# Kernel tuning notes

Measured on AMD Instinct MI355X. Metric: run time of the kernel, lower is better.

The kernel has to match this reference:

```python
import jax, jax.numpy as jnp
import numpy as np

HEADS = 8
NEG_SLOPE = 0.2


def _layer_norm(x, g, b, eps=1e-5):
    mu = x.mean(-1, keepdims=True)
    var = ((x - mu) ** 2).mean(-1, keepdims=True)
    return (x - mu) / jnp.sqrt(var + eps) * g + b


def setup_inputs() -> dict:
    key = jax.random.key(0)
    ks = jax.random.split(key, 24)
    N, E, H, L = 512, 260000, 256, 4
    s = 0.05
    return dict(
        x=jax.random.normal(ks[0], (N, 1), jnp.float32),
        edge_index=jax.random.randint(ks[1], (2, E), 0, N),
        edge_attr=jax.random.uniform(ks[2], (E, 3), jnp.float32),
        emb_W=jax.random.normal(ks[3], (1, H)) * s,
        emb_b=jnp.zeros((H,)),
        Wl=jax.random.normal(ks[4], (L, H, H)) * s,
        bl=jnp.zeros((L, H)),
        Wr=jax.random.normal(ks[5], (L, H, H)) * s,
        br=jnp.zeros((L, H)),
        We=jax.random.normal(ks[6], (L, 3, H)) * s,
        att=jax.random.normal(ks[7], (L, HEADS, H // HEADS)) * s,
        gb=jnp.zeros((L, H)),
        ln_g=jnp.ones((L, H)),
        ln_b=jnp.zeros((L, H)),
        p1_W=jax.random.normal(ks[8], (2 * H, H)) * s,
        p1_b=jnp.zeros((H,)),
        p2_W=jax.random.normal(ks[9], (H, H // 2)) * s,
        p2_b=jnp.zeros((H // 2,)),
        p3_W=jax.random.normal(ks[10], (H // 2, 1)) * s,
        p3_b=jnp.zeros((1,)),
        v1_W=jax.random.normal(ks[11], (2 * H, H)) * s,
        v1_b=jnp.zeros((H,)),
        v2_W=jax.random.normal(ks[12], (H, 1)) * s,
        v2_b=jnp.zeros((1,)),
        coupling=jnp.asarray(1.0, jnp.float32),
    )


def reference(x, edge_index, edge_attr, emb_W, emb_b, Wl, bl, Wr, br, We, att,
              gb, ln_g, ln_b, p1_W, p1_b, p2_W, p2_b, p3_W, p3_b,
              v1_W, v1_b, v2_W, v2_b, coupling):
    N = x.shape[0]
    E = edge_attr.shape[0]
    L = Wl.shape[0]
    C = Wl.shape[-1] // HEADS
    src, dst = edge_index[0], edge_index[1]

    # PyG GATv2Conv adds self-loops with edge_attr fill_value='mean'
    # (mean of incoming edge_attr per destination node).
    sums = jax.ops.segment_sum(edge_attr, dst, num_segments=N)
    cnt = jax.ops.segment_sum(jnp.ones((E,), edge_attr.dtype), dst, num_segments=N)
    self_attr = sums / jnp.maximum(cnt, 1.0)[:, None]
    loop = jnp.arange(N)
    src_f = jnp.concatenate([src, loop])            # [E+N]
    dst_f = jnp.concatenate([dst, loop])
    ea_f = jnp.concatenate([edge_attr, self_attr])  # [E+N, 3]

    h = x @ emb_W + emb_b                           # [N, H]
    for l in range(L):
        res = h
        xl = (h @ Wl[l] + bl[l]).reshape(N, HEADS, C)
        xr = (h @ Wr[l] + br[l]).reshape(N, HEADS, C)
        ee = (ea_f @ We[l]).reshape(-1, HEADS, C)
        # GATv2 scoring: leaky_relu(x_l[src]+x_r[dst]+edge) . att
        m = jax.nn.leaky_relu(xl[src_f] + xr[dst_f] + ee, NEG_SLOPE)
        alpha = jnp.einsum('ehc,hc->eh', m, att[l])
        amax = jax.ops.segment_max(alpha, dst_f, num_segments=N)
        alpha = jnp.exp(alpha - amax[dst_f])
        denom = jax.ops.segment_sum(alpha, dst_f, num_segments=N)
        alpha = alpha / denom[dst_f]
        out = jax.ops.segment_sum(xl[src_f] * alpha[..., None], dst_f,
                                  num_segments=N).reshape(N, HEADS * C) + gb[l]
        h = jax.nn.relu(_layer_norm(out + res, ln_g[l], ln_b[l]))

    # graph-level representation (single graph, batch=None branch)
    graph_repr = jnp.concatenate([h.mean(0, keepdims=True),
                                  h.max(0, keepdims=True)], axis=1)  # [1, 2H]

    # all-pairs edge representations (i < j)
    iu, ju = jnp.triu_indices(N, k=1)
    er = jnp.concatenate([h[iu], h[ju]], axis=1)    # [N(N-1)/2, 2H]
    p = jax.nn.relu(er @ p1_W + p1_b)
    p = jax.nn.relu(p @ p2_W + p2_b)
    policy_logits = (p @ p3_W + p3_b).squeeze(-1)   # [N(N-1)/2]

    v = jax.nn.relu(graph_repr @ v1_W + v1_b)
    value = (v @ v2_W + v2_b).squeeze(-1)           # [1]

    # Potts energy: per-color degree-squared approximation of triangles
    colors = jnp.argmax(edge_attr, axis=1)
    energy = jnp.asarray(0.0, h.dtype)
    for c in (1, 2):
        w = (colors == c).astype(h.dtype)
        deg = (jax.ops.segment_sum(w, src, num_segments=N)
               + jax.ops.segment_sum(w, dst, num_segments=N))
        energy = energy + (deg ** 2).sum() / (2.0 * N)
    energy = energy * coupling

    return policy_logits, value, energy
```

## Files before the change

kernel.cpp:

```cpp
#include <hip/hip_runtime.h>
#include <math.h>

#define HDIM 256
#define NHEADS 8
#define NEG 0.2f
#define SEG 4
#define STRIDE 768

typedef float f32x4 __attribute__((ext_vector_type(4)));
typedef _Float16 f16x8 __attribute__((ext_vector_type(8)));
typedef __fp16 fp16v2 __attribute__((ext_vector_type(2)));

union H8 { f16x8 v8; fp16v2 v2[4]; _Float16 h[8]; };

#if __has_builtin(__builtin_amdgcn_fdot2)
#define FDOT2(a, b, c) __builtin_amdgcn_fdot2((a), (b), (c), false)
#else
__device__ __forceinline__ float FDOT2(fp16v2 a, fp16v2 b, float c) {
  return fmaf((float)a[1], (float)b[1], fmaf((float)a[0], (float)b[0], c));
}
#endif

__global__ __launch_bounds__(256) void zero_k(int* __restrict__ p) {
  p[blockIdx.x * 256 + threadIdx.x] = 0;
}

__global__ __launch_bounds__(256) void build_csr(
    const int* __restrict__ ei, const float* __restrict__ ea, int E, int CH,
    int* __restrict__ rcnt, float* __restrict__ asum, int* __restrict__ dcol,
    float4* __restrict__ csr) {
  __shared__ int   lcnt[512];
  __shared__ float ls0[512], ls1[512], ls2[512];
  __shared__ int   lcol[1024];
  __shared__ int   lbase[512];
  int t = threadIdx.x, b = blockIdx.x;
  for (int n = t; n < 512; n += 256) {
    lcnt[n] = 0; ls0[n] = 0.f; ls1[n] = 0.f; ls2[n] = 0.f;
    lcol[n] = 0; lcol[512 + n] = 0;
  }
  __syncthreads();
  int e0 = b * CH, e1 = min(E, e0 + CH);

  int nd[4], ns[4], slot[4];
  float va0[4], va1[4], va2[4];
#pragma unroll
  for (int k = 0; k < 4; ++k) {
    int e = e0 + t + (k << 8);
    bool v = e < e1;
    if (v) {
      int src = ei[e], dst = ei[E + e];
      float a0 = ea[3*e], a1 = ea[3*e+1], a2 = ea[3*e+2];
      nd[k] = dst; ns[k] = src; va0[k] = a0; va1[k] = a1; va2[k] = a2;
      slot[k] = atomicAdd(&lcnt[dst], 1);
      atomicAdd(&ls0[dst], a0);
      atomicAdd(&ls1[dst], a1);
      atomicAdd(&ls2[dst], a2);
      int idx = 0; float best = a0;
      if (a1 > best) { best = a1; idx = 1; }
      if (a2 > best) { idx = 2; }
      if (idx) {
        int o = (idx - 1) << 9;
        atomicAdd(&lcol[o + src], 1);
        atomicAdd(&lcol[o + dst], 1);
      }
    } else {
      nd[k] = -1;
    }
  }
  __syncthreads();
  for (int n = t; n < 512; n += 256) {
    int c = lcnt[n];
    if (c) {
      lbase[n] = atomicAdd(&rcnt[n], c);
      atomicAdd(&asum[n],        ls0[n]);
      atomicAdd(&asum[512 + n],  ls1[n]);
      atomicAdd(&asum[1024 + n], ls2[n]);
    }
    int c0 = lcol[n], c1 = lcol[512 + n];
    if (c0) atomicAdd(&dcol[n], c0);
    if (c1) atomicAdd(&dcol[512 + n], c1);
  }
  __syncthreads();
#pragma unroll
  for (int k = 0; k < 4; ++k) {
    if (nd[k] >= 0) {
      int pos = nd[k]*STRIDE + 1 + lbase[nd[k]] + slot[k];
      csr[pos] = make_float4(va0[k], va1[k], va2[k], __int_as_float(ns[k]));
    }
  }
}

__global__ __launch_bounds__(512) void csr_finish(
    const int* __restrict__ rcnt, const float* __restrict__ asum,
    const int* __restrict__ dcol, int N,
    float4* __restrict__ csr, const float* __restrict__ coupling,
    float* __restrict__ eout) {
  int t = threadIdx.x;
  float e = 0.f;
  if (t < N) {
    int c = rcnt[t];
    float inv = 1.f / fmaxf((float)c, 1.f);
    csr[(size_t)t*STRIDE] = make_float4(asum[t]*inv, asum[512 + t]*inv,
                                        asum[1024 + t]*inv, __int_as_float(t));
    float d1 = (float)dcol[t], d2 = (float)dcol[512 + t];
    e = d1*d1 + d2*d2;
  }
#pragma unroll
  for (int off = 1; off < 64; off <<= 1) e += __shfl_xor(e, off);
  __shared__ float wred[8];
  if ((t & 63) == 0) wred[t >> 6] = e;
  __syncthreads();
  if (t == 0) {
    float s = 0.f;
#pragma unroll
    for (int i = 0; i < 8; ++i) s += wred[i];
    eout[0] = coupling[0] * s / (2.f * (float)N);
  }
}

__global__ __launch_bounds__(256) void w_prep_all(
    const float* __restrict__ Wl, const float* __restrict__ Wr,
    const float* __restrict__ p1W, const float* __restrict__ W2,
    unsigned short* __restrict__ dst, unsigned short* __restrict__ W2h) {
  int gid = blockIdx.x * 256 + threadIdx.x;
  if (gid < 10*65536) {
    int s = gid >> 16, e = gid & 65535;
    int k = e >> 8, n = e & 255;
    const float* src = (s < 4) ? (Wl + (size_t)s*65536)
                     : (s < 8) ? (Wr + (size_t)(s-4)*65536)
                               : (p1W + (size_t)(s-8)*65536);
    int c = k >> 5, quad = (k >> 3) & 3, kj = k & 7;
    int nt = n >> 4, nl = n & 15;
    int lane = quad*16 + nl;
    _Float16 hv = (_Float16)src[(size_t)k*256 + n];
    dst[(size_t)s*65536 + ((nt*8 + c)*512 + lane*8 + kj)] = *(unsigned short*)&hv;
  } else {
    int e = gid - 10*65536;
    int k = e >> 7, n = e & 127;
    int c = k >> 5, kq = (k >> 3) & 3, kj = k & 7;
    int nt = n >> 4, nl = n & 15;
    int lane = kq*16 + nl;
    _Float16 hv = (_Float16)W2[(size_t)k*128 + n];
    W2h[(size_t)(((c*8 + nt)*64 + lane)*8 + kj)] = *(unsigned short*)&hv;
  }
}

__global__ __launch_bounds__(256) void dual_gemm_mfma(
    const float* __restrict__ Hm,
    const float* __restrict__ x, const float* __restrict__ embW,
    const float* __restrict__ embb,
    const unsigned short* __restrict__ W1h, const unsigned short* __restrict__ W2h,
    const float* __restrict__ b1, const float* __restrict__ b2,
    float* __restrict__ o1, unsigned short* __restrict__ o1h,
    float* __restrict__ o2, unsigned short* __restrict__ o2h) {
  int bx = blockIdx.x, by = blockIdx.y;
  int t = threadIdx.x, w = t >> 6, l = t & 63;
  int quad = l >> 4, nl = l & 15;
  int mt = bx*4 + w;

  const unsigned short* Wh; const float* bias; float* o; unsigned short* oh; int nt;
  bool first = (by < 16);
  if (first) { Wh = W1h; bias = b1; o = o1; oh = o1h; nt = by; }
  else       { Wh = W2h; bias = b2; o = o2; oh = o2h; nt = by - 16; }

  int row = mt*16 + nl;
  const float* Ar = Hm ? (Hm + (size_t)row*HDIM + quad*8) : nullptr;
  float xm = Hm ? 0.f : x[row];
  f32x4 acc = (f32x4){0.f, 0.f, 0.f, 0.f};

#pragma unroll
  for (int c = 0; c < 8; ++c) {
    float4 a0, a1;
    if (Hm) {
      a0 = *(const float4*)(Ar + c*32);
      a1 = *(const float4*)(Ar + c*32 + 4);
    } else {
      int kb = c*32 + quad*8;
      float4 e0 = *(const float4*)(embW + kb);
      float4 e1 = *(const float4*)(embW + kb + 4);
      float4 c0 = *(const float4*)(embb + kb);
      float4 c1 = *(const float4*)(embb + kb + 4);
      a0 = make_float4(fmaf(xm, e0.x, c0.x), fmaf(xm, e0.y, c0.y),
                       fmaf(xm, e0.z, c0.z), fmaf(xm, e0.w, c0.w));
      a1 = make_float4(fmaf(xm, e1.x, c1.x), fmaf(xm, e1.y, c1.y),
                       fmaf(xm, e1.z, c1.z), fmaf(xm, e1.w, c1.w));
    }
    union { f16x8 v8; fp16v2 v2[4]; } u;
    u.v2[0] = __builtin_amdgcn_cvt_pkrtz(a0.x, a0.y);
    u.v2[1] = __builtin_amdgcn_cvt_pkrtz(a0.z, a0.w);
    u.v2[2] = __builtin_amdgcn_cvt_pkrtz(a1.x, a1.y);
    u.v2[3] = __builtin_amdgcn_cvt_pkrtz(a1.z, a1.w);
    f16x8 bfrag = *(const f16x8*)(Wh + (size_t)((nt*8 + c)*512 + l*8));
    acc = __builtin_amdgcn_mfma_f32_16x16x32_f16(u.v8, bfrag, acc, 0, 0, 0);
  }

  int colg = nt*16 + nl;
  float bv = bias ? bias[colg] : 0.f;
#pragma unroll
  for (int r = 0; r < 4; ++r) {
    float val = acc[r] + bv;
    size_t idx = (size_t)(mt*16 + quad*4 + r)*HDIM + colg;
    if (o) o[idx] = val;
    if (oh) {
      _Float16 hv = (_Float16)val;
      oh[idx] = *(unsigned short*)&hv;
    }
  }
}

__global__ __launch_bounds__(256) void attn_gather(
    const unsigned short* __restrict__ xlh, const unsigned short* __restrict__ xrh,
    const float4* __restrict__ csr, const int* __restrict__ rcnt,
    const float* __restrict__ We, const float* __restrict__ att,
    float* __restrict__ pm, float* __restrict__ pl, float* __restrict__ pacc) {
  int nb = blockIdx.x;
  int n = nb >> 2, sgm = nb & (SEG - 1);
  int t = threadIdx.x;
  int g = t >> 5, l = t & 31, hd = l >> 2, qd = l & 3;
  int cb = hd*32 + qd*8;

  union H8 w0u, w1u, w2u, avu;
#pragma unroll
  for (int p = 0; p < 4; ++p) {
    w0u.v2[p] = __builtin_amdgcn_cvt_pkrtz(We[cb + 2*p],          We[cb + 2*p + 1]);
    w1u.v2[p] = __builtin_amdgcn_cvt_pkrtz(We[HDIM + cb + 2*p],   We[HDIM + cb + 2*p + 1]);
    w2u.v2[p] = __builtin_amdgcn_cvt_pkrtz(We[2*HDIM + cb + 2*p], We[2*HDIM + cb + 2*p + 1]);
    avu.v2[p] = __builtin_amdgcn_cvt_pkrtz(att[cb + 2*p],         att[cb + 2*p + 1]);
  }
  f16x8 xr8 = *(const f16x8*)(xrh + (size_t)n*HDIM + cb);

  int base = n * STRIDE;
  int len = rcnt[n] + 1;
  int s0 = base + ((len * sgm) >> 2);
  int s1 = base + ((len * (sgm + 1)) >> 2);

  float mh = -INFINITY, lh = 0.f;
  float acc[8] = {0.f,0.f,0.f,0.f,0.f,0.f,0.f,0.f};

  int idx = s0 + g;
  if (idx < s1) {
    float4 rec = csr[idx];
    int idx1 = idx + 8;
    float4 rec1 = csr[idx1 < s1 ? idx1 : base];
    union H8 cur, nxt;
    cur.v8 = *(const f16x8*)(xlh + (size_t)__float_as_int(rec.w)*HDIM + cb);
    while (idx < s1) {
      int idx2 = idx1 + 8;
      float4 rec2 = csr[idx2 < s1 ? idx2 : base];
      nxt.v8 = *(const f16x8*)(xlh +
                (size_t)__float_as_int(rec1.w)*HDIM + cb);
      _Float16 hx = (_Float16)rec.x, hy = (_Float16)rec.y, hz = (_Float16)rec.z;
      f16x8 s = cur.v8 + xr8;
      s = s + w0u.v8 * hx;
      s = s + w1u.v8 * hy;
      s = s + w2u.v8 * hz;
      union H8 m;
      m.v8 = __builtin_elementwise_max(s, s * (_Float16)NEG);
      float partial = FDOT2(m.v2[3], avu.v2[3],
                      FDOT2(m.v2[2], avu.v2[2],
                      FDOT2(m.v2[1], avu.v2[1],
                      FDOT2(m.v2[0], avu.v2[0], 0.f))));
      partial += __shfl_xor(partial, 1);
      partial += __shfl_xor(partial, 2);
      if (partial - mh > 8.f) {
        float sc = __expf(mh - partial);
        lh *= sc;
#pragma unroll
        for (int j = 0; j < 8; ++j) acc[j] *= sc;
        mh = partial;
      }
      float pw = __expf(partial - mh);
      lh += pw;
#pragma unroll
      for (int j = 0; j < 8; ++j) acc[j] = fmaf(pw, (float)cur.h[j], acc[j]);
      rec = rec1; rec1 = rec2; cur.v8 = nxt.v8;
      idx = idx1; idx1 = idx2;
    }
  }

  __shared__ float lacc[8][HDIM];
  __shared__ float lm[8][NHEADS];
  __shared__ float llv[8][NHEADS];
#pragma unroll
  for (int j = 0; j < 8; ++j) lacc[g][cb + j] = acc[j];
  if (qd == 0) { lm[g][hd] = mh; llv[g][hd] = lh; }
  __syncthreads();

  int c = t, hh = c >> 5;
  float M = -INFINITY;
#pragma unroll
  for (int g2 = 0; g2 < 8; ++g2) M = fmaxf(M, lm[g2][hh]);
  float L = 0.f, o = 0.f;
#pragma unroll
  for (int g2 = 0; g2 < 8; ++g2) {
    float e2 = __expf(lm[g2][hh] - M);
    L = fmaf(llv[g2][hh], e2, L);
    o = fmaf(lacc[g2][c], e2, o);
  }
  pacc[(size_t)nb*HDIM + c] = o;
  if ((c & 31) == 0) {
    pm[nb*NHEADS + hh] = M;
    pl[nb*NHEADS + hh] = L;
  }
}

__global__ __launch_bounds__(256) void attn_merge(
    const float* __restrict__ pm, const float* __restrict__ pl,
    const float* __restrict__ pacc,
    const float* __restrict__ gb, const float* __restrict__ lng,
    const float* __restrict__ lnb,
    const float* __restrict__ h_in,
    const float* __restrict__ x, const float* __restrict__ embW,
    const float* __restrict__ embb,
    float* __restrict__ h_out) {
  int n = blockIdx.x, t = threadIdx.x;
  int c = t, hh = c >> 5;
  float M = -INFINITY;
#pragma unroll
  for (int s = 0; s < SEG; ++s) M = fmaxf(M, pm[(n*SEG + s)*NHEADS + hh]);
  float L = 0.f, o = 0.f;
#pragma unroll
  for (int s = 0; s < SEG; ++s) {
    float e2 = __expf(pm[(n*SEG + s)*NHEADS + hh] - M);
    L = fmaf(pl[(n*SEG + s)*NHEADS + hh], e2, L);
    o = fmaf(pacc[(size_t)(n*SEG + s)*HDIM + c], e2, o);
  }
  float hi = h_in ? h_in[(size_t)n*HDIM + c] : fmaf(x[n], embW[c], embb[c]);
  float val = o / L + gb[c] + hi;

  float s1 = val, s2 = val * val;
#pragma unroll
  for (int off = 1; off < 64; off <<= 1) {
    s1 += __shfl_xor(s1, off);
    s2 += __shfl_xor(s2, off);
  }
  __shared__ float rs1[4], rs2[4];
  if ((t & 63) == 0) { rs1[t >> 6] = s1; rs2[t >> 6] = s2; }
  __syncthreads();
  float S1 = rs1[0] + rs1[1] + rs1[2] + rs1[3];
  float S2 = rs2[0] + rs2[1] + rs2[2] + rs2[3];
  float mu = S1 * (1.f/HDIM);
  float var = S2 * (1.f/HDIM) - mu * mu;
  float y = (val - mu) * rsqrtf(var + 1e-5f);
  y = fmaf(y, lng[c], lnb[c]);
  h_out[(size_t)n*HDIM + c] = fmaxf(y, 0.f);
}

__global__ __launch_bounds__(256, 4) void pair_mfma_kernel(
    const unsigned short* __restrict__ Ah, const unsigned short* __restrict__ Bh,
    const unsigned short* __restrict__ W2h,
    const float* __restrict__ b2, const float* __restrict__ W3,
    const float* __restrict__ b3, float* __restrict__ out, int N) {
  int bb = blockIdx.x;
  int half = bb & 1;
  int b = bb >> 1, ti = 0, rem = 32;
  while (b >= rem) { b -= rem; ti++; rem--; }
  int tj = ti + b;
  int i0 = ti * 16 + half * 8;
  int j0 = tj * 16;

  int t = threadIdx.x;
  int w = t >> 6, l = t & 63;
  int quad = l >> 4, nl = l & 15;

  float b2v[8], w3v[8];
#pragma unroll
  for (int nt = 0; nt < 8; ++nt) {
    b2v[nt] = b2[nt*16 + nl];
    w3v[nt] = W3[nt*16 + nl];
  }

  const unsigned short* Brow = Bh + (size_t)(j0 + nl) * HDIM;
  const unsigned short* Arow0 = Ah + (size_t)(i0 + w*2) * HDIM;
  const f16x8 zv = {};

  f32x4 acc[2][8];
#pragma unroll
  for (int a2 = 0; a2 < 2; ++a2)
#pragma unroll
    for (int nt = 0; nt < 8; ++nt) acc[a2][nt] = (f32x4){0.f,0.f,0.f,0.f};

  for (int c = 0; c < 8; ++c) {
    int kb = c*32 + quad*8;
    f16x8 bv = *(const f16x8*)(Brow + kb);

    f16x8 afrag[2];
#pragma unroll
    for (int a2 = 0; a2 < 2; ++a2) {
      f16x8 av = *(const f16x8*)(Arow0 + (size_t)a2*HDIM + kb);
      afrag[a2] = __builtin_elementwise_max(av + bv, zv);
    }

#pragma unroll
    for (int nt = 0; nt < 8; ++nt) {
      f16x8 bfrag = *(const f16x8*)(W2h + (size_t)(((c*8 + nt)*64 + l) * 8));
#pragma unroll
      for (int a2 = 0; a2 < 2; ++a2)
        acc[a2][nt] = __builtin_amdgcn_mfma_f32_16x16x32_f16(
            afrag[a2], bfrag, acc[a2][nt], 0, 0, 0);
    }
  }

  float b3v = b3[0];
#pragma unroll
  for (int a2 = 0; a2 < 2; ++a2) {
    int i = i0 + w*2 + a2;
#pragma unroll
    for (int r = 0; r < 4; ++r) {
      float s = 0.f;
#pragma unroll
      for (int nt = 0; nt < 8; ++nt)
        s = fmaf(fmaxf(acc[a2][nt][r] + b2v[nt], 0.f), w3v[nt], s);
      s += __shfl_xor(s, 1);
      s += __shfl_xor(s, 2);
      s += __shfl_xor(s, 4);
      s += __shfl_xor(s, 8);
      if (nl == 0) {
        int j = j0 + quad*4 + r;
        if (i < j)
          out[(size_t)i*(2*N - i - 1)/2 + (j - i - 1)] = s + b3v;
      }
    }
  }
}

__global__ __launch_bounds__(256) void pool_kernel(
    const float* __restrict__ h, float* __restrict__ psums,
    float* __restrict__ pmaxs) {
  int g = blockIdx.x, t = threadIdx.x;
  float s = 0.f, m = -INFINITY;
#pragma unroll
  for (int r = 0; r < 16; ++r) {
    float v = h[(size_t)(g*16 + r)*HDIM + t];
    s += v; m = fmaxf(m, v);
  }
  psums[g*HDIM + t] = s;
  pmaxs[g*HDIM + t] = m;
}

__global__ __launch_bounds__(256) void value1_kernel(
    const float* __restrict__ psums, const float* __restrict__ pmaxs,
    const float* __restrict__ v1W, float* __restrict__ vpart, int N) {
  int b = blockIdx.x, t = threadIdx.x;
  int k0 = b * 16;
  int kk = t >> 4, g = t & 15;
  __shared__ float repr16[16];
  int k = k0 + kk;
  float v;
  if (k < HDIM) {
    v = psums[g*HDIM + k] + psums[(g + 16)*HDIM + k];
    v += __shfl_xor(v, 1); v += __shfl_xor(v, 2);
    v += __shfl_xor(v, 4); v += __shfl_xor(v, 8);
    if (g == 0) repr16[kk] = v / (float)N;
  } else {
    int kc = k - HDIM;
    v = fmaxf(pmaxs[g*HDIM + kc], pmaxs[(g + 16)*HDIM + kc]);
    v = fmaxf(v, __shfl_xor(v, 1)); v = fmaxf(v, __shfl_xor(v, 2));
    v = fmaxf(v, __shfl_xor(v, 4)); v = fmaxf(v, __shfl_xor(v, 8));
    if (g == 0) repr16[kk] = v;
  }
  __syncthreads();
  float pv = 0.f;
#pragma unroll
  for (int q = 0; q < 16; ++q)
    pv = fmaf(repr16[q], v1W[(size_t)(k0 + q)*HDIM + t], pv);
  vpart[b*HDIM + t] = pv;
}

__global__ __launch_bounds__(256) void value2_kernel(
    const float* __restrict__ vpart, const float* __restrict__ v1b,
    const float* __restrict__ v2W, const float* __restrict__ v2b,
    float* __restrict__ out) {
  int t = threadIdx.x;
  float a = 0.f;
#pragma unroll
  for (int g = 0; g < 32; ++g) a += vpart[g*HDIM + t];
  a = fmaxf(a + v1b[t], 0.f);
  float pv = a * v2W[t];
#pragma unroll
  for (int off = 1; off < 64; off <<= 1) pv += __shfl_xor(pv, off);
  __shared__ float wsum[4];
  if ((t & 63) == 0) wsum[t >> 6] = pv;
  __syncthreads();
  if (t == 0) out[0] = wsum[0] + wsum[1] + wsum[2] + wsum[3] + v2b[0];
}

extern "C" void kernel_launch(void* const* d_in, const int* in_sizes, int n_in,
                              void* d_out, int out_size, void* d_ws, size_t ws_size,
                              hipStream_t stream) {
  const float* x    = (const float*)d_in[0];
  const int*   ei   = (const int*)  d_in[1];
  const float* ea   = (const float*)d_in[2];
  const float* embW = (const float*)d_in[3];
  const float* embb = (const float*)d_in[4];
  const float* Wl   = (const float*)d_in[5];
  const float* bl   = (const float*)d_in[6];
  const float* Wr   = (const float*)d_in[7];
  const float* br   = (const float*)d_in[8];
  const float* We   = (const float*)d_in[9];
  const float* att  = (const float*)d_in[10];
  const float* gb   = (const float*)d_in[11];
  const float* lng  = (const float*)d_in[12];
  const float* lnb  = (const float*)d_in[13];
  const float* p1W  = (const float*)d_in[14];
  const float* p1b  = (const float*)d_in[15];
  const float* p2W  = (const float*)d_in[16];
  const float* p2b  = (const float*)d_in[17];
  const float* p3W  = (const float*)d_in[18];
  const float* p3b  = (const float*)d_in[19];
  const float* v1W  = (const float*)d_in[20];
  const float* v1b  = (const float*)d_in[21];
  const float* v2W  = (const float*)d_in[22];
  const float* v2b  = (const float*)d_in[23];
  const float* coup = (const float*)d_in[24];

  int N = in_sizes[0];
  int E = in_sizes[2] / 3;
  float* out = (float*)d_out;
  size_t P = (size_t)N*(N-1)/2;

  char* w = (char*)d_ws;
  int*    rcnt = (int*)   (w + 0);
  float*  asum = (float*) (w + 2048);
  int*    dcol = (int*)   (w + 8192);
  float*  plS  = (float*) (w + 12288);
  float*  plM  = (float*) (w + 45056);
  float*  vprt = (float*) (w + 77824);
  float4* csr  = (float4*)(w + 110592);
  float* hA  = (float*)(w + 6402048);
  float* hB  = (float*)(w + 6926336);
  unsigned short* xlh = (unsigned short*)(w + 7450624);
  unsigned short* xrh = (unsigned short*)(w + 7712768);
  unsigned short* Abh = (unsigned short*)(w + 7974912);
  unsigned short* Bbh = (unsigned short*)(w + 8237056);
  unsigned short* W2h = (unsigned short*)(w + 8499200);
  unsigned short* Whall = (unsigned short*)(w + 8564736);
  float*  pmv  = (float*) (w + 9875456);
  float*  plv  = (float*) (w + 9940992);
  float*  pacc = (float*) (w + 10006528);

  zero_k<<<12, 256, 0, stream>>>(rcnt);
  int nbB = (E + 1023) >> 10;
  build_csr<<<nbB, 256, 0, stream>>>(ei, ea, E, 1024, rcnt, asum, dcol, csr);
  csr_finish<<<1, 512, 0, stream>>>(rcnt, asum, dcol, N, csr, coup, out + P + 1);
  w_prep_all<<<2688, 256, 0, stream>>>(Wl, Wr, p1W, p2W, Whall, W2h);

  float* hin = nullptr;
  float* hout = hB;
  for (int l = 0; l < 4; ++l) {
    dual_gemm_mfma<<<dim3(8, 32), 256, 0, stream>>>(hin, x, embW, embb,
        Whall + (size_t)l*65536, Whall + (size_t)(4 + l)*65536,
        bl + l*HDIM, br + l*HDIM,
        (float*)nullptr, xlh, (float*)nullptr, xrh);
    attn_gather<<<N*SEG, 256, 0, stream>>>(xlh, xrh, csr, rcnt,
        We + (size_t)l*3*HDIM, att + (size_t)l*HDIM, pmv, plv, pacc);
    attn_merge<<<N, 256, 0, stream>>>(pmv, plv, pacc,
        gb + (size_t)l*HDIM, lng + (size_t)l*HDIM, lnb + (size_t)l*HDIM,
        hin, x, embW, embb, hout);
    hin = hout;
    hout = (hout == hB) ? hA : hB;
  }

  dual_gemm_mfma<<<dim3(8, 32), 256, 0, stream>>>(hin, x, embW, embb,
      Whall + (size_t)8*65536, Whall + (size_t)9*65536,
      p1b, (const float*)nullptr,
      (float*)nullptr, Abh, (float*)nullptr, Bbh);

  pair_mfma_kernel<<<1056, 256, 0, stream>>>(Abh, Bbh, W2h, p2b, p3W, p3b, out, N);

  pool_kernel<<<32, 256, 0, stream>>>(hin, plS, plM);
  value1_kernel<<<32, 256, 0, stream>>>(plS, plM, v1W, vprt, N);
  value2_kernel<<<1, 256, 0, stream>>>(vprt, v1b, v2W, v2b, out + P);
}
```

Before: 298.1 us.

## Fuse whole pipeline into persistent megakernel with software grid barriers

Replaces the sequence of roughly twenty kernel launches with one persistent kernel of 512 blocks. Stages are separated by an atomic-counter grid barrier, and independent work (CSR build with weight prep, CSR finish with the first GEMM, pooling with the final GEMM) is co-scheduled within a stage. The attention gather no longer splits each node into 4 segments plus a separate merge; one block now handles a whole node with a deeper prefetch pipeline and applies LayerNorm inline. This removes launch gaps and the partial-result round trips, but gives less parallelism per node in the gather, and the barrier relies on all 512 blocks being resident at once.

```diff
diff --git a/kernel.cpp b/kernel.cpp
--- a/kernel.cpp
+++ b/kernel.cpp
@@ -4,8 +4,8 @@
 #define HDIM 256
 #define NHEADS 8
 #define NEG 0.2f
-#define SEG 4
 #define STRIDE 768
+#define GRID 512
 
 typedef float f32x4 __attribute__((ext_vector_type(4)));
 typedef _Float16 f16x8 __attribute__((ext_vector_type(8)));
@@ -25,29 +25,39 @@
   p[blockIdx.x * 256 + threadIdx.x] = 0;
 }
 
-__global__ __launch_bounds__(256) void build_csr(
-    const int* __restrict__ ei, const float* __restrict__ ea, int E, int CH,
-    int* __restrict__ rcnt, float* __restrict__ asum, int* __restrict__ dcol,
-    float4* __restrict__ csr) {
-  __shared__ int   lcnt[512];
-  __shared__ float ls0[512], ls1[512], ls2[512];
-  __shared__ int   lcol[1024];
-  __shared__ int   lbase[512];
-  int t = threadIdx.x, b = blockIdx.x;
+__device__ __forceinline__ void gbar(int* bar, int target) {
+  __syncthreads();
+  if (threadIdx.x == 0) {
+    __hip_atomic_fetch_add(bar, 1, __ATOMIC_ACQ_REL, __HIP_MEMORY_SCOPE_AGENT);
+    while (__hip_atomic_load(bar, __ATOMIC_RELAXED, __HIP_MEMORY_SCOPE_AGENT) < target)
+      __builtin_amdgcn_s_sleep(2);
+    (void)__hip_atomic_load(bar, __ATOMIC_ACQUIRE, __HIP_MEMORY_SCOPE_AGENT);
+  }
+  __syncthreads();
+}
+
+__device__ __forceinline__ void build_work(int b, const int* ei, const float* ea,
+    int E, int* rcnt, float* asum, int* dcol, float4* csr, char* SMEM) {
+  int*   lcnt = (int*)SMEM;
+  float* ls0  = (float*)(SMEM + 2048);
+  float* ls1  = (float*)(SMEM + 4096);
+  float* ls2  = (float*)(SMEM + 6144);
+  int*   lcol = (int*)(SMEM + 8192);
+  int*   lbase= (int*)(SMEM + 12288);
+  int t = threadIdx.x;
   for (int n = t; n < 512; n += 256) {
     lcnt[n] = 0; ls0[n] = 0.f; ls1[n] = 0.f; ls2[n] = 0.f;
     lcol[n] = 0; lcol[512 + n] = 0;
   }
   __syncthreads();
-  int e0 = b * CH, e1 = min(E, e0 + CH);
+  int e0 = b << 10, e1 = min(E, e0 + 1024);
 
   int nd[4], ns[4], slot[4];
   float va0[4], va1[4], va2[4];
 #pragma unroll
   for (int k = 0; k < 4; ++k) {
     int e = e0 + t + (k << 8);
-    bool v = e < e1;
-    if (v) {
+    if (e < e1) {
       int src = ei[e], dst = ei[E + e];
       float a0 = ea[3*e], a1 = ea[3*e+1], a2 = ea[3*e+2];
       nd[k] = dst; ns[k] = src; va0[k] = a0; va1[k] = a1; va2[k] = a2;
@@ -90,39 +100,10 @@
   }
 }
 
-__global__ __launch_bounds__(512) void csr_finish(
-    const int* __restrict__ rcnt, const float* __restrict__ asum,
-    const int* __restrict__ dcol, int N,
-    float4* __restrict__ csr, const float* __restrict__ coupling,
-    float* __restrict__ eout) {
-  int t = threadIdx.x;
-  float e = 0.f;
-  if (t < N) {
-    int c = rcnt[t];
-    float inv = 1.f / fmaxf((float)c, 1.f);
-    csr[(size_t)t*STRIDE] = make_float4(asum[t]*inv, asum[512 + t]*inv,
-                                        asum[1024 + t]*inv, __int_as_float(t));
-    float d1 = (float)dcol[t], d2 = (float)dcol[512 + t];
-    e = d1*d1 + d2*d2;
-  }
-#pragma unroll
-  for (int off = 1; off < 64; off <<= 1) e += __shfl_xor(e, off);
-  __shared__ float wred[8];
-  if ((t & 63) == 0) wred[t >> 6] = e;
-  __syncthreads();
-  if (t == 0) {
-    float s = 0.f;
-#pragma unroll
-    for (int i = 0; i < 8; ++i) s += wred[i];
-    eout[0] = coupling[0] * s / (2.f * (float)N);
-  }
-}
-
-__global__ __launch_bounds__(256) void w_prep_all(
-    const float* __restrict__ Wl, const float* __restrict__ Wr,
-    const float* __restrict__ p1W, const float* __restrict__ W2,
-    unsigned short* __restrict__ dst, unsigned short* __restrict__ W2h) {
-  int gid = blockIdx.x * 256 + threadIdx.x;
+__device__ __forceinline__ void wprep_work(int wid, const float* Wl,
+    const float* Wr, const float* p1W, const float* W2,
+    unsigned short* dst, unsigned short* W2h) {
+  int gid = wid * 256 + (int)threadIdx.x;
   if (gid < 10*65536) {
     int s = gid >> 16, e = gid & 65535;
     int k = e >> 8, n = e & 255;
@@ -145,23 +126,41 @@
   }
 }
 
-__global__ __launch_bounds__(256) void dual_gemm_mfma(
-    const float* __restrict__ Hm,
-    const float* __restrict__ x, const float* __restrict__ embW,
-    const float* __restrict__ embb,
-    const unsigned short* __restrict__ W1h, const unsigned short* __restrict__ W2h,
-    const float* __restrict__ b1, const float* __restrict__ b2,
-    float* __restrict__ o1, unsigned short* __restrict__ o1h,
-    float* __restrict__ o2, unsigned short* __restrict__ o2h) {
-  int bx = blockIdx.x, by = blockIdx.y;
+__device__ __forceinline__ void csrfin_work(int half, const int* rcnt,
+    const float* asum, const int* dcol, int N, float4* csr, float* epart,
+    char* SMEM) {
+  float* er = (float*)SMEM;
+  int t = threadIdx.x;
+  int n = half*256 + t;
+  float e = 0.f;
+  if (n < N) {
+    int c = rcnt[n];
+    float inv = 1.f / fmaxf((float)c, 1.f);
+    csr[(size_t)n*STRIDE] = make_float4(asum[n]*inv, asum[512 + n]*inv,
+                                        asum[1024 + n]*inv, __int_as_float(n));
+    float d1 = (float)dcol[n], d2 = (float)dcol[512 + n];
+    e = d1*d1 + d2*d2;
+  }
+#pragma unroll
+  for (int off = 1; off < 64; off <<= 1) e += __shfl_xor(e, off);
+  if ((t & 63) == 0) er[t >> 6] = e;
+  __syncthreads();
+  if (t == 0) epart[half] = er[0] + er[1] + er[2] + er[3];
+}
+
+__device__ __forceinline__ void gemm_work(int wid, const float* Hm,
+    const float* x, const float* embW, const float* embb,
+    const unsigned short* W1h, const unsigned short* W2h_,
+    const float* b1, const float* b2,
+    unsigned short* o1h, unsigned short* o2h) {
+  int bx = wid & 7, by = wid >> 3;
   int t = threadIdx.x, w = t >> 6, l = t & 63;
   int quad = l >> 4, nl = l & 15;
   int mt = bx*4 + w;
 
-  const unsigned short* Wh; const float* bias; float* o; unsigned short* oh; int nt;
-  bool first = (by < 16);
-  if (first) { Wh = W1h; bias = b1; o = o1; oh = o1h; nt = by; }
-  else       { Wh = W2h; bias = b2; o = o2; oh = o2h; nt = by - 16; }
+  const unsigned short* Wh; const float* bias; unsigned short* oh; int nt;
+  if (by < 16) { Wh = W1h; bias = b1; oh = o1h; nt = by; }
+  else         { Wh = W2h_; bias = b2; oh = o2h; nt = by - 16; }
 
   int row = mt*16 + nl;
   const float* Ar = Hm ? (Hm + (size_t)row*HDIM + quad*8) : nullptr;
@@ -200,22 +199,29 @@
   for (int r = 0; r < 4; ++r) {
     float val = acc[r] + bv;
     size_t idx = (size_t)(mt*16 + quad*4 + r)*HDIM + colg;
-    if (o) o[idx] = val;
-    if (oh) {
-      _Float16 hv = (_Float16)val;
-      oh[idx] = *(unsigned short*)&hv;
-    }
-  }
-}
-
-__global__ __launch_bounds__(256) void attn_gather(
-    const unsigned short* __restrict__ xlh, const unsigned short* __restrict__ xrh,
-    const float4* __restrict__ csr, const int* __restrict__ rcnt,
-    const float* __restrict__ We, const float* __restrict__ att,
-    float* __restrict__ pm, float* __restrict__ pl, float* __restrict__ pacc) {
-  int nb = blockIdx.x;
-  int n = nb >> 2, sgm = nb & (SEG - 1);
+    _Float16 hv = (_Float16)val;
+    oh[idx] = *(unsigned short*)&hv;
+  }
+}
+
+__device__ __forceinline__ void gather_merge_work(int n,
+    const unsigned short* xlh, const unsigned short* xrh,
+    const float4* csr, const int* rcnt,
+    const float* We, const float* att,
+    const float* gb, const float* lng, const float* lnb,
+    const float* h_in, const float* x, const float* embW, const float* embb,
+    float* h_out, const float* epart, const float* coup, float* eout,
+    int N, char* SMEM) {
+  float* lacc = (float*)SMEM;
+  float* lm   = (float*)(SMEM + 8192);
+  float* llv  = (float*)(SMEM + 8448);
+  float* rs1  = (float*)(SMEM + 8704);
+  float* rs2  = (float*)(SMEM + 8720);
+
   int t = threadIdx.x;
+  if (eout && t == 0)
+    eout[0] = coup[0] * (epart[0] + epart[1]) / (2.f * (float)N);
+
   int g = t >> 5, l = t & 31, hd = l >> 2, qd = l & 3;
   int cb = hd*32 + qd*8;
 
@@ -230,25 +236,25 @@
   f16x8 xr8 = *(const f16x8*)(xrh + (size_t)n*HDIM + cb);
 
   int base = n * STRIDE;
-  int len = rcnt[n] + 1;
-  int s0 = base + ((len * sgm) >> 2);
-  int s1 = base + ((len * (sgm + 1)) >> 2);
+  int send = base + rcnt[n] + 1;
 
   float mh = -INFINITY, lh = 0.f;
   float acc[8] = {0.f,0.f,0.f,0.f,0.f,0.f,0.f,0.f};
 
-  int idx = s0 + g;
-  if (idx < s1) {
-    float4 rec = csr[idx];
-    int idx1 = idx + 8;
-    float4 rec1 = csr[idx1 < s1 ? idx1 : base];
-    union H8 cur, nxt;
+  int idx = base + g;
+  if (idx < send) {
+    int i1 = idx + 8, i2 = idx + 16;
+    float4 rec  = csr[idx];
+    float4 rec1 = csr[i1 < send ? i1 : base];
+    float4 rec2 = csr[i2 < send ? i2 : base];
+    union H8 cur, nxt, nx2;
     cur.v8 = *(const f16x8*)(xlh + (size_t)__float_as_int(rec.w)*HDIM + cb);
-    while (idx < s1) {
-      int idx2 = idx1 + 8;
-      float4 rec2 = csr[idx2 < s1 ? idx2 : base];
-      nxt.v8 = *(const f16x8*)(xlh +
-                (size_t)__float_as_int(rec1.w)*HDIM + cb);
+    nxt.v8 = *(const f16x8*)(xlh + (size_t)__float_as_int(rec1.w)*HDIM + cb);
+    while (idx < send) {
+      int i3 = i2 + 8;
+      float4 rec3 = csr[i3 < send ? i3 : base];
+      nx2.v8 = *(const f16x8*)(xlh +
+                (size_t)__float_as_int(rec2.w)*HDIM + cb);
       _Float16 hx = (_Float16)rec.x, hy = (_Float16)rec.y, hz = (_Float16)rec.z;
       f16x8 s = cur.v8 + xr8;
       s = s + w0u.v8 * hx;
@@ -273,69 +279,38 @@
       lh += pw;
 #pragma unroll
       for (int j = 0; j < 8; ++j) acc[j] = fmaf(pw, (float)cur.h[j], acc[j]);
-      rec = rec1; rec1 = rec2; cur.v8 = nxt.v8;
-      idx = idx1; idx1 = idx2;
-    }
-  }
-
-  __shared__ float lacc[8][HDIM];
-  __shared__ float lm[8][NHEADS];
-  __shared__ float llv[8][NHEADS];
-#pragma unroll
-  for (int j = 0; j < 8; ++j) lacc[g][cb + j] = acc[j];
-  if (qd == 0) { lm[g][hd] = mh; llv[g][hd] = lh; }
+      rec = rec1; rec1 = rec2; rec2 = rec3;
+      cur.v8 = nxt.v8; nxt.v8 = nx2.v8;
+      idx = i1; i1 = i2; i2 = i3;
+    }
+  }
+
+#pragma unroll
+  for (int j = 0; j < 8; ++j) lacc[g*HDIM + cb + j] = acc[j];
+  if (qd == 0) { lm[g*NHEADS + hd] = mh; llv[g*NHEADS + hd] = lh; }
   __syncthreads();
 
   int c = t, hh = c >> 5;
   float M = -INFINITY;
 #pragma unroll
-  for (int g2 = 0; g2 < 8; ++g2) M = fmaxf(M, lm[g2][hh]);
+  for (int g2 = 0; g2 < 8; ++g2) M = fmaxf(M, lm[g2*NHEADS + hh]);
   float L = 0.f, o = 0.f;
 #pragma unroll
   for (int g2 = 0; g2 < 8; ++g2) {
-    float e2 = __expf(lm[g2][hh] - M);
-    L = fmaf(llv[g2][hh], e2, L);
-    o = fmaf(lacc[g2][c], e2, o);
-  }
-  pacc[(size_t)nb*HDIM + c] = o;
-  if ((c & 31) == 0) {
-    pm[nb*NHEADS + hh] = M;
-    pl[nb*NHEADS + hh] = L;
-  }
-}
-
-__global__ __launch_bounds__(256) void attn_merge(
-    const float* __restrict__ pm, const float* __restrict__ pl,
-    const float* __restrict__ pacc,
-    const float* __restrict__ gb, const float* __restrict__ lng,
-    const float* __restrict__ lnb,
-    const float* __restrict__ h_in,
-    const float* __restrict__ x, const float* __restrict__ embW,
-    const float* __restrict__ embb,
-    float* __restrict__ h_out) {
-  int n = blockIdx.x, t = threadIdx.x;
-  int c = t, hh = c >> 5;
-  float M = -INFINITY;
-#pragma unroll
-  for (int s = 0; s < SEG; ++s) M = fmaxf(M, pm[(n*SEG + s)*NHEADS + hh]);
-  float L = 0.f, o = 0.f;
-#pragma unroll
-  for (int s = 0; s < SEG; ++s) {
-    float e2 = __expf(pm[(n*SEG + s)*NHEADS + hh] - M);
-    L = fmaf(pl[(n*SEG + s)*NHEADS + hh], e2, L);
-    o = fmaf(pacc[(size_t)(n*SEG + s)*HDIM + c], e2, o);
+    float e2 = __expf(lm[g2*NHEADS + hh] - M);
+    L = fmaf(llv[g2*NHEADS + hh], e2, L);
+    o = fmaf(lacc[g2*HDIM + c], e2, o);
   }
   float hi = h_in ? h_in[(size_t)n*HDIM + c] : fmaf(x[n], embW[c], embb[c]);
   float val = o / L + gb[c] + hi;
 
-  float s1 = val, s2 = val * val;
+  float vs = val, vq = val * val;
 #pragma unroll
   for (int off = 1; off < 64; off <<= 1) {
-    s1 += __shfl_xor(s1, off);
-    s2 += __shfl_xor(s2, off);
-  }
-  __shared__ float rs1[4], rs2[4];
-  if ((t & 63) == 0) { rs1[t >> 6] = s1; rs2[t >> 6] = s2; }
+    vs += __shfl_xor(vs, off);
+    vq += __shfl_xor(vq, off);
+  }
+  if ((t & 63) == 0) { rs1[t >> 6] = vs; rs2[t >> 6] = vq; }
   __syncthreads();
   float S1 = rs1[0] + rs1[1] + rs1[2] + rs1[3];
   float S2 = rs2[0] + rs2[1] + rs2[2] + rs2[3];
@@ -346,12 +321,10 @@
   h_out[(size_t)n*HDIM + c] = fmaxf(y, 0.f);
 }
 
-__global__ __launch_bounds__(256, 4) void pair_mfma_kernel(
-    const unsigned short* __restrict__ Ah, const unsigned short* __restrict__ Bh,
-    const unsigned short* __restrict__ W2h,
-    const float* __restrict__ b2, const float* __restrict__ W3,
-    const float* __restrict__ b3, float* __restrict__ out, int N) {
-  int bb = blockIdx.x;
+__device__ __forceinline__ void pair_work(int bb,
+    const unsigned short* Ah, const unsigned short* Bh,
+    const unsigned short* W2h, const float* b2, const float* W3,
+    const float* b3, float* out, int N) {
   int half = bb & 1;
   int b = bb >> 1, ti = 0, rem = 32;
   while (b >= rem) { b -= rem; ti++; rem--; }
@@ -424,10 +397,9 @@
   }
 }
 
-__global__ __launch_bounds__(256) void pool_kernel(
-    const float* __restrict__ h, float* __restrict__ psums,
-    float* __restrict__ pmaxs) {
-  int g = blockIdx.x, t = threadIdx.x;
+__device__ __forceinline__ void pool_work(int g, const float* h,
+    float* psums, float* pmaxs) {
+  int t = threadIdx.x;
   float s = 0.f, m = -INFINITY;
 #pragma unroll
   for (int r = 0; r < 16; ++r) {
@@ -438,51 +410,119 @@
   pmaxs[g*HDIM + t] = m;
 }
 
-__global__ __launch_bounds__(256) void value1_kernel(
-    const float* __restrict__ psums, const float* __restrict__ pmaxs,
-    const float* __restrict__ v1W, float* __restrict__ vpart, int N) {
-  int b = blockIdx.x, t = threadIdx.x;
-  int k0 = b * 16;
-  int kk = t >> 4, g = t & 15;
-  __shared__ float repr16[16];
-  int k = k0 + kk;
-  float v;
-  if (k < HDIM) {
-    v = psums[g*HDIM + k] + psums[(g + 16)*HDIM + k];
-    v += __shfl_xor(v, 1); v += __shfl_xor(v, 2);
-    v += __shfl_xor(v, 4); v += __shfl_xor(v, 8);
-    if (g == 0) repr16[kk] = v / (float)N;
-  } else {
-    int kc = k - HDIM;
-    v = fmaxf(pmaxs[g*HDIM + kc], pmaxs[(g + 16)*HDIM + kc]);
-    v = fmaxf(v, __shfl_xor(v, 1)); v = fmaxf(v, __shfl_xor(v, 2));
-    v = fmaxf(v, __shfl_xor(v, 4)); v = fmaxf(v, __shfl_xor(v, 8));
-    if (g == 0) repr16[kk] = v;
-  }
-  __syncthreads();
-  float pv = 0.f;
-#pragma unroll
-  for (int q = 0; q < 16; ++q)
-    pv = fmaf(repr16[q], v1W[(size_t)(k0 + q)*HDIM + t], pv);
-  vpart[b*HDIM + t] = pv;
-}
-
-__global__ __launch_bounds__(256) void value2_kernel(
-    const float* __restrict__ vpart, const float* __restrict__ v1b,
+__device__ __forceinline__ void value_work(int q, const float* psums,
+    const float* pmaxs, const float* v1W, const float* v1b,
+    const float* v2W, float* out_val, int N, char* SMEM) {
+  float* repr = (float*)SMEM;
+  float* vred = (float*)(SMEM + 2048);
+  int t = threadIdx.x;
+  float s = 0.f, m = -INFINITY;
+#pragma unroll 8
+  for (int g = 0; g < 32; ++g) {
+    s += psums[g*HDIM + t];
+    m = fmaxf(m, pmaxs[g*HDIM + t]);
+  }
+  repr[t] = s / (float)N;
+  repr[256 + t] = m;
+  __syncthreads();
+  int cc = t & 63, kk = t >> 6;
+  int c = q*64 + cc;
+  float p = 0.f;
+#pragma unroll 8
+  for (int k = kk*128; k < kk*128 + 128; ++k)
+    p = fmaf(repr[k], v1W[(size_t)k*HDIM + c], p);
+  vred[kk*64 + cc] = p;
+  __syncthreads();
+  if (t < 64) {
+    float a = vred[t] + vred[64 + t] + vred[128 + t] + vred[192 + t] + v1b[c];
+    a = fmaxf(a, 0.f);
+    float pd = a * v2W[c];
+#pragma unroll
+    for (int off = 1; off < 64; off <<= 1) pd += __shfl_xor(pd, off);
+    if (t == 0) atomicAdd(out_val, pd);
+  }
+}
+
+__global__ __launch_bounds__(256, 2) void mega(
+    const float* __restrict__ x, const int* __restrict__ ei,
+    const float* __restrict__ ea,
+    const float* __restrict__ embW, const float* __restrict__ embb,
+    const float* __restrict__ Wl, const float* __restrict__ bl,
+    const float* __restrict__ Wr, const float* __restrict__ br,
+    const float* __restrict__ We, const float* __restrict__ att,
+    const float* __restrict__ gb, const float* __restrict__ lng,
+    const float* __restrict__ lnb,
+    const float* __restrict__ p1W, const float* __restrict__ p1b,
+    const float* __restrict__ p2W, const float* __restrict__ p2b,
+    const float* __restrict__ p3W, const float* __restrict__ p3b,
+    const float* __restrict__ v1W, const float* __restrict__ v1b,
     const float* __restrict__ v2W, const float* __restrict__ v2b,
-    float* __restrict__ out) {
-  int t = threadIdx.x;
-  float a = 0.f;
-#pragma unroll
-  for (int g = 0; g < 32; ++g) a += vpart[g*HDIM + t];
-  a = fmaxf(a + v1b[t], 0.f);
-  float pv = a * v2W[t];
-#pragma unroll
-  for (int off = 1; off < 64; off <<= 1) pv += __shfl_xor(pv, off);
-  __shared__ float wsum[4];
-  if ((t & 63) == 0) wsum[t >> 6] = pv;
-  __syncthreads();
-  if (t == 0) out[0] = wsum[0] + wsum[1] + wsum[2] + wsum[3] + v2b[0];
+    const float* __restrict__ coup,
+    int* rcnt, float* asum, int* dcol, float* epart,
+    float4* csr, float* hA, float* hB,
+    unsigned short* xlh, unsigned short* xrh,
+    unsigned short* Abh, unsigned short* Bbh,
+    unsigned short* W2h, unsigned short* Whall,
+    float* psums, float* pmaxs, int* bar,
+    float* out, int N, int E) {
+  __shared__ __align__(16) char SMEM[14336];
+  size_t P = (size_t)N*(N-1)/2;
+  int ph = 0;
+
+  {
+    int WB = (E + 1023) >> 10;
+    for (int wid = blockIdx.x; wid < WB + 2688; wid += GRID) {
+      if (wid < WB) build_work(wid, ei, ea, E, rcnt, asum, dcol, csr, SMEM);
+      else          wprep_work(wid - WB, Wl, Wr, p1W, p2W, Whall, W2h);
+    }
+  }
+  ++ph; gbar(bar, ph * GRID);
+
+  for (int wid = blockIdx.x; wid < 258; wid += GRID) {
+    if (wid < 2) csrfin_work(wid, rcnt, asum, dcol, N, csr, epart, SMEM);
+    else gemm_work(wid - 2, nullptr, x, embW, embb,
+                   Whall, Whall + (size_t)4*65536, bl, br, xlh, xrh);
+  }
+  ++ph; gbar(bar, ph * GRID);
+
+  const float* hin = nullptr;
+  float* hout = hB;
+  for (int l = 0; l < 4; ++l) {
+    if (l) {
+      for (int wid = blockIdx.x; wid < 256; wid += GRID)
+        gemm_work(wid, hin, x, embW, embb,
+                  Whall + (size_t)l*65536, Whall + (size_t)(4 + l)*65536,
+                  bl + l*HDIM, br + l*HDIM, xlh, xrh);
+      ++ph; gbar(bar, ph * GRID);
+    }
+    for (int wid = blockIdx.x; wid < N; wid += GRID)
+      gather_merge_work(wid, xlh, xrh, csr, rcnt,
+                        We + (size_t)l*3*HDIM, att + (size_t)l*HDIM,
+                        gb + l*HDIM, lng + l*HDIM, lnb + l*HDIM,
+                        hin, x, embW, embb, hout,
+                        epart, coup,
+                        (l == 0 && wid == 0) ? (out + P + 1) : nullptr,
+                        N, SMEM);
+    ++ph; gbar(bar, ph * GRID);
+    hin = hout;
+    hout = (hout == hB) ? hA : hB;
+  }
+
+  for (int wid = blockIdx.x; wid < 288; wid += GRID) {
+    if (wid < 256) gemm_work(wid, hin, x, embW, embb,
+                             Whall + (size_t)8*65536, Whall + (size_t)9*65536,
+                             p1b, nullptr, Abh, Bbh);
+    else {
+      pool_work(wid - 256, hin, psums, pmaxs);
+      if (wid == 256 && threadIdx.x == 0) out[P] = v2b[0];
+    }
+  }
+  ++ph; gbar(bar, ph * GRID);
+
+  for (int wid = blockIdx.x; wid < 1060; wid += GRID) {
+    if (wid < 4) value_work(wid, psums, pmaxs, v1W, v1b, v2W, out + P, N, SMEM);
+    else pair_work(wid - 4, Abh, Bbh, W2h, p2b, p3W, p3b, out, N);
+  }
 }
 
 extern "C" void kernel_launch(void* const* d_in, const int* in_sizes, int n_in,
@@ -517,58 +557,29 @@
   int N = in_sizes[0];
   int E = in_sizes[2] / 3;
   float* out = (float*)d_out;
-  size_t P = (size_t)N*(N-1)/2;
 
   char* w = (char*)d_ws;
-  int*    rcnt = (int*)   (w + 0);
-  float*  asum = (float*) (w + 2048);
-  int*    dcol = (int*)   (w + 8192);
-  float*  plS  = (float*) (w + 12288);
-  float*  plM  = (float*) (w + 45056);
-  float*  vprt = (float*) (w + 77824);
-  float4* csr  = (float4*)(w + 110592);
-  float* hA  = (float*)(w + 6402048);
-  float* hB  = (float*)(w + 6926336);
-  unsigned short* xlh = (unsigned short*)(w + 7450624);
-  unsigned short* xrh = (unsigned short*)(w + 7712768);
-  unsigned short* Abh = (unsigned short*)(w + 7974912);
-  unsigned short* Bbh = (unsigned short*)(w + 8237056);
-  unsigned short* W2h = (unsigned short*)(w + 8499200);
-  unsigned short* Whall = (unsigned short*)(w + 8564736);
-  float*  pmv  = (float*) (w + 9875456);
-  float*  plv  = (float*) (w + 9940992);
-  float*  pacc = (float*) (w + 10006528);
-
-  zero_k<<<12, 256, 0, stream>>>(rcnt);
-  int nbB = (E + 1023) >> 10;
-  build_csr<<<nbB, 256, 0, stream>>>(ei, ea, E, 1024, rcnt, asum, dcol, csr);
-  csr_finish<<<1, 512, 0, stream>>>(rcnt, asum, dcol, N, csr, coup, out + P + 1);
-  w_prep_all<<<2688, 256, 0, stream>>>(Wl, Wr, p1W, p2W, Whall, W2h);
-
-  float* hin = nullptr;
-  float* hout = hB;
-  for (int l = 0; l < 4; ++l) {
-    dual_gemm_mfma<<<dim3(8, 32), 256, 0, stream>>>(hin, x, embW, embb,
-        Whall + (size_t)l*65536, Whall + (size_t)(4 + l)*65536,
-        bl + l*HDIM, br + l*HDIM,
-        (float*)nullptr, xlh, (float*)nullptr, xrh);
-    attn_gather<<<N*SEG, 256, 0, stream>>>(xlh, xrh, csr, rcnt,
-        We + (size_t)l*3*HDIM, att + (size_t)l*HDIM, pmv, plv, pacc);
-    attn_merge<<<N, 256, 0, stream>>>(pmv, plv, pacc,
-        gb + (size_t)l*HDIM, lng + (size_t)l*HDIM, lnb + (size_t)l*HDIM,
-        hin, x, embW, embb, hout);
-    hin = hout;
-    hout = (hout == hB) ? hA : hB;
-  }
-
-  dual_gemm_mfma<<<dim3(8, 32), 256, 0, stream>>>(hin, x, embW, embb,
-      Whall + (size_t)8*65536, Whall + (size_t)9*65536,
-      p1b, (const float*)nullptr,
-      (float*)nullptr, Abh, (float*)nullptr, Bbh);
-
-  pair_mfma_kernel<<<1056, 256, 0, stream>>>(Abh, Bbh, W2h, p2b, p3W, p3b, out, N);
-
-  pool_kernel<<<32, 256, 0, stream>>>(hin, plS, plM);
-  value1_kernel<<<32, 256, 0, stream>>>(plS, plM, v1W, vprt, N);
-  value2_kernel<<<1, 256, 0, stream>>>(vprt, v1b, v2W, v2b, out + P);
-}
+  int*    bar  = (int*)   (w + 0);
+  int*    rcnt = (int*)   (w + 256);
+  float*  asum = (float*) (w + 2304);
+  int*    dcol = (int*)   (w + 8448);
+  float*  epart= (float*) (w + 12544);
+  float*  psums= (float*) (w + 12800);
+  float*  pmaxs= (float*) (w + 45568);
+  float4* csr  = (float4*)(w + 78336);
+  float*  hA   = (float*) (w + 6369792);
+  float*  hB   = (float*) (w + 6894080);
+  unsigned short* xlh   = (unsigned short*)(w + 7418368);
+  unsigned short* xrh   = (unsigned short*)(w + 7680512);
+  unsigned short* Abh   = (unsigned short*)(w + 7942656);
+  unsigned short* Bbh   = (unsigned short*)(w + 8204800);
+  unsigned short* W2h   = (unsigned short*)(w + 8466944);
+  unsigned short* Whall = (unsigned short*)(w + 8532480);
+
+  zero_k<<<13, 256, 0, stream>>>((int*)w);
+  mega<<<GRID, 256, 0, stream>>>(
+      x, ei, ea, embW, embb, Wl, bl, Wr, br, We, att, gb, lng, lnb,
+      p1W, p1b, p2W, p2b, p3W, p3b, v1W, v1b, v2W, v2b, coup,
+      rcnt, asum, dcol, epart, csr, hA, hB, xlh, xrh, Abh, Bbh,
+      W2h, Whall, psums, pmaxs, bar, out, N, E);
+}
```

After: 743.8 us. 2.49x slower.
